# Kernel tuning notes

Measured on AMD Instinct MI355X. Metric: run time of the kernel, lower is better.

The kernel has to match this reference:

```python
import jax, jax.numpy as jnp
import numpy as np
import math

B, N, P, S, C, NC = 8, 20000, 256, 32, 256, 18


def setup_inputs() -> dict:
    key = jax.random.key(0)
    ks = jax.random.split(key, 20)
    w = lambda k, shape: jax.random.normal(k, shape, jnp.float32) * 0.02
    return {
        "xyz": jax.random.normal(ks[0], (B, N, 3), jnp.float32),
        "features": jax.random.normal(ks[1], (B, C, N), jnp.float32),
        "boxes_size": jax.random.uniform(ks[2], (B, P, 3), jnp.float32, 0.2, 1.5),
        "boxes_label": jax.random.normal(ks[3], (B, P, NC), jnp.float32),
        "ts": jax.random.uniform(ks[4], (B,), jnp.float32) * 1000.0,
        "inds": jax.random.randint(ks[5], (B, P), 0, N, jnp.int32),
        # SharedMLP (259 -> 128 -> 128 -> 128), bn=False so conv1x1+bias+ReLU
        "mw0": w(ks[6], (128, C + 3)), "mb0": jnp.zeros((128,), jnp.float32),
        "mw1": w(ks[7], (128, 128)), "mb1": jnp.zeros((128,), jnp.float32),
        "mw2": w(ks[8], (128, 128)), "mb2": jnp.zeros((128,), jnp.float32),
        # label SharedMLP (18+128 -> 256 -> 256 -> 256)
        "lw0": w(ks[9], (256, NC + 128)), "lb0": jnp.zeros((256,), jnp.float32),
        "lw1": w(ks[10], (256, 256)), "lb1": jnp.zeros((256,), jnp.float32),
        "lw2": w(ks[11], (256, 256)), "lb2": jnp.zeros((256,), jnp.float32),
        # time_mlp: sinusoid(128) -> 512 -> GELU -> 512 ; block: SiLU -> 256
        "tw0": w(ks[12], (512, 128)), "tb0": jnp.zeros((512,), jnp.float32),
        "tw1": w(ks[13], (512, 512)), "tb1": jnp.zeros((512,), jnp.float32),
        "bw": w(ks[14], (256, 512)), "bb": jnp.zeros((256,), jnp.float32),
        # time_mlp_label: sinusoid(256) -> 1024 -> GELU -> 1024 ; block: SiLU -> 512
        "tlw0": w(ks[15], (1024, 256)), "tlb0": jnp.zeros((1024,), jnp.float32),
        "tlw1": w(ks[16], (1024, 1024)), "tlb1": jnp.zeros((1024,), jnp.float32),
        "blw": w(ks[17], (512, 1024)), "blb": jnp.zeros((512,), jnp.float32),
    }


def _sinusoid(t, dim):
    half = dim // 2
    freqs = jnp.exp(jnp.arange(half, dtype=jnp.float32) * (-(math.log(10000.0) / (half - 1))))
    e = t[:, None] * freqs[None, :]
    return jnp.concatenate([jnp.sin(e), jnp.cos(e)], axis=-1)


def _film(feat, ts, w0, b0, w1, b1, bw, bb, dim):
    # feat: [B, D, P]; replicates torch repeat_interleave/chunk/reshape exactly
    temb = jax.nn.gelu(_sinusoid(ts, dim) @ w0.T + b0, approximate=False) @ w1.T + b1
    ss = jax.nn.silu(temb) @ bw.T + bb          # [B, 2D]
    ss = jnp.repeat(ss, P, axis=0)              # [B*P, 2D]
    scale, shift = jnp.split(ss, 2, axis=1)
    scale = scale.reshape(-1, P)
    shift = shift.reshape(-1, P)
    f = feat.reshape(-1, P)
    return (f * (scale + 1.0) + shift).reshape(feat.shape[0], -1, P)


def reference(xyz, features, boxes_size, boxes_label, ts, inds,
              mw0, mb0, mw1, mb1, mw2, mb2,
              lw0, lb0, lw1, lb1, lw2, lb2,
              tw0, tb0, tw1, tb1, bw, bb,
              tlw0, tlb0, tlw1, tlb1, blw, blb):
    # gather proposal centers
    new_xyz = jnp.take_along_axis(xyz, inds[:, :, None], axis=1)        # [B,P,3]
    # axis-aligned box containment (the hull corners are an AABB: center +/- size/2)
    half = boxes_size * 0.5
    inside = jnp.all(jnp.abs(xyz[:, None, :, :] - new_xyz[:, :, None, :]) <= half[:, :, None, :], axis=-1)  # [B,P,N]
    # deterministic with-replacement sampling of in-box points: in-box indices first (stable sort), then cycle
    order = jnp.argsort(jnp.logical_not(inside), axis=-1)               # [B,P,N]
    count = jnp.maximum(inside.sum(axis=-1), 1)                          # [B,P]
    pos = jnp.arange(S, dtype=count.dtype)[None, None, :] % count[:, :, None]
    idx = jnp.take_along_axis(order, pos, axis=-1)                       # [B,P,S]
    b_idx = jnp.arange(B)[:, None, None]
    gxyz = xyz[b_idx, idx] - new_xyz[:, :, None, :]                      # [B,P,S,3]
    gfeat = jnp.transpose(features, (0, 2, 1))[b_idx, idx]               # [B,P,S,C]
    g = jnp.concatenate([gxyz, gfeat], axis=-1)                          # [B,P,S,3+C]
    act = lambda x, w, b: jax.nn.relu(jnp.einsum('bpsc,oc->bpso', x, w) + b)
    h = act(act(act(g, mw0, mb0), mw1, mb1), mw2, mb2)                   # [B,P,S,128]
    nf = h.max(axis=2)                                                   # [B,P,128] (max-pool over nsample)
    nf_t = jnp.transpose(nf, (0, 2, 1))                                  # [B,128,P]
    new_features = _film(nf_t, ts, tw0, tb0, tw1, tb1, bw, bb, 128)
    # label branch
    li = jnp.concatenate([boxes_label, nf], axis=-1)                     # [B,P,18+128]
    act2 = lambda x, w, b: jax.nn.relu(jnp.einsum('bpc,oc->bpo', x, w) + b)
    lf = act2(act2(act2(li, lw0, lb0), lw1, lb1), lw2, lb2)              # [B,P,256]
    lf_t = jnp.transpose(lf, (0, 2, 1))                                  # [B,256,P]
    label_feature = _film(lf_t, ts, tlw0, tlb0, tlw1, tlb1, blw, blb, 256)
    return (new_xyz, new_features, label_feature, inds)
```

## Files before the change

### kernel.cpp

```cpp
#include <hip/hip_runtime.h>
#include <math.h>

#define BB 8
#define NN 20000
#define PP 256
#define SSAMP 32
#define CC 256

typedef unsigned short u16;
typedef unsigned int u32;
typedef __attribute__((ext_vector_type(8))) short short8;
typedef __attribute__((ext_vector_type(4))) float f32x4;

__device__ __forceinline__ float b2f(u16 u) {
    union { u32 i; float f; } x; x.i = ((u32)u) << 16; return x.f;
}
__device__ __forceinline__ u16 f2b(float f) {
    union { float f; u32 i; } x; x.f = f;
    u32 i = x.i;
    i += 0x7fffu + ((i >> 16) & 1u);
    return (u16)(i >> 16);
}
__device__ __forceinline__ float rnd_bf(float f) { return b2f(f2b(f)); }
__device__ __forceinline__ float geluf(float x) {
    return 0.5f * x * (1.0f + erff(x * 0.7071067811865476f));
}
__device__ __forceinline__ float siluf(float x) {
    return x / (1.0f + expf(-x));
}
__device__ __forceinline__ f32x4 fz4() { f32x4 z = {0.f,0.f,0.f,0.f}; return z; }

__device__ __forceinline__ float ldf(const void* p, size_t i, int f32f) {
    return f32f ? ((const float*)p)[i] : b2f(((const u16*)p)[i]);
}
__device__ __forceinline__ u16 ldw(const void* p, size_t i, int f32f) {
    return f32f ? f2b(((const float*)p)[i]) : ((const u16*)p)[i];
}

__device__ __forceinline__ int detect_f32d(const void* xyz) {
    int lane = threadIdx.x & 63;
    u16 u = ((const u16*)xyz)[(size_t)lane * 7496];
    int e = (u >> 7) & 0xFF;
    bool inR = (e >= 0x70) && (e <= 0x85);
    unsigned long long m = __ballot(inR);
    return (__popcll(m) < 48) ? 1 : 0;
}

__device__ __forceinline__ void repack_body(int f32f, int rb, int tid,
        const void* mw0, const void* mw1, const void* mw2,
        const void* lw0, const void* lw1, const void* lw2,
        const void* mb0, const void* mb1, const void* mb2,
        const void* lb0, const void* lb1, const void* lb2,
        u16* __restrict__ W0p, u16* __restrict__ W1p, u16* __restrict__ W2p,
        u16* __restrict__ L0p, u16* __restrict__ L1p, u16* __restrict__ L2p,
        float* __restrict__ biasF) {
    int i = rb * 256 + tid;
    if (i < 36864) {
        int o = i / 288, c = i % 288;
        u16 v = 0;
        if (c < 256) v = ldw(mw0, o * 259 + 3 + c, f32f);
        else if (c < 259) v = ldw(mw0, o * 259 + (c - 256), f32f);
        W0p[i] = v;
    } else if (i < 53248) {
        W1p[i - 36864] = ldw(mw1, i - 36864, f32f);
    } else if (i < 69632) {
        W2p[i - 53248] = ldw(mw2, i - 53248, f32f);
    } else if (i < 110592) {
        int j = i - 69632;
        int o = j / 160, c = j % 160;
        L0p[j] = (c < 146) ? ldw(lw0, o * 146 + c, f32f) : (u16)0;
    } else if (i < 176128) {
        L1p[i - 110592] = ldw(lw1, i - 110592, f32f);
    } else if (i < 241664) {
        L2p[i - 176128] = ldw(lw2, i - 176128, f32f);
    } else if (i < 242816) {
        int j = i - 241664;
        float v;
        if (j < 128) v = ldf(mb0, j, f32f);
        else if (j < 256) v = ldf(mb1, j - 128, f32f);
        else if (j < 384) v = ldf(mb2, j - 256, f32f);
        else if (j < 640) v = ldf(lb0, j - 384, f32f);
        else if (j < 896) v = ldf(lb1, j - 640, f32f);
        else v = ldf(lb2, j - 896, f32f);
        biasF[j] = v;
    }
}

__device__ __forceinline__ void transpose_body(int f32f, const void* __restrict__ feat,
        u16* __restrict__ featT, int n0i, int c0i, int bz, int b0, int tid,
        u16 (*tile)[66]) {
    int c0 = c0i * 64, n0 = n0i * 64;
    int b = b0 + bz;
    const size_t fb = (size_t)b * CC * NN;
    const size_t tb = (size_t)bz * NN * CC;
    if (n0 + 64 <= NN) {
        int n4 = tid & 15, ci = tid >> 4;
        if (f32f) {
            #pragma unroll
            for (int pass = 0; pass < 4; pass++) {
                int c = pass * 16 + ci;
                const float* src = (const float*)feat + fb + (size_t)(c0 + c) * NN + n0 + n4 * 4;
                float4 v = *(const float4*)src;
                tile[c][n4 * 4 + 0] = f2b(v.x);
                tile[c][n4 * 4 + 1] = f2b(v.y);
                tile[c][n4 * 4 + 2] = f2b(v.z);
                tile[c][n4 * 4 + 3] = f2b(v.w);
            }
        } else {
            #pragma unroll
            for (int pass = 0; pass < 4; pass++) {
                int c = pass * 16 + ci;
                const u16* src = (const u16*)feat + fb + (size_t)(c0 + c) * NN + n0 + n4 * 4;
                ushort4 v = *(const ushort4*)src;
                tile[c][n4 * 4 + 0] = v.x;
                tile[c][n4 * 4 + 1] = v.y;
                tile[c][n4 * 4 + 2] = v.z;
                tile[c][n4 * 4 + 3] = v.w;
            }
        }
        __syncthreads();
        int c4 = tid & 15, ni = tid >> 4;
        #pragma unroll
        for (int pass = 0; pass < 4; pass++) {
            int n = pass * 16 + ni;
            ushort4 o;
            o.x = tile[c4 * 4 + 0][n];
            o.y = tile[c4 * 4 + 1][n];
            o.z = tile[c4 * 4 + 2][n];
            o.w = tile[c4 * 4 + 3][n];
            *(ushort4*)(featT + tb + (size_t)(n0 + n) * CC + c0 + c4 * 4) = o;
        }
    } else {
        int tx = tid & 63, ty = tid >> 6;
        for (int i = 0; i < 16; i++) {
            int cl = ty * 16 + i;
            int n = n0 + tx;
            if (n < NN) tile[cl][tx] = ldw(feat, fb + (size_t)(c0 + cl) * NN + n, f32f);
        }
        __syncthreads();
        for (int i = 0; i < 16; i++) {
            int nl = ty * 16 + i;
            int n = n0 + nl;
            if (n < NN) featT[tb + (size_t)n * CC + c0 + tx] = tile[tx][nl];
        }
    }
}

template<int ACT, int SRC>
__device__ __forceinline__ void lin_body(int f32f, const void* __restrict__ xin,
        const void* __restrict__ W, const void* __restrict__ bias,
        float* __restrict__ out, int K, int O, int rb, int tid, float* xs) {
    if (SRC == 2) {
        const float* X = (const float*)xin;
        for (int i = tid; i < 8 * K; i += 256) xs[i] = X[i];
    } else {
        const int half = (SRC == 0) ? 64 : 128;
        const int dim = half * 2;
        const float cst = (SRC == 0) ? (logf(10000.f) / 63.f) : (logf(10000.f) / 127.f);
        for (int i = tid; i < 8 * dim; i += 256) {
            int b = i / dim, j = i % dim;
            float t = ldf(xin, b, f32f);
            int jj = (j < half) ? j : (j - half);
            float e = t * expf(-(float)jj * cst);
            xs[i] = (j < half) ? sinf(e) : cosf(e);
        }
    }
    __syncthreads();
    int lane = tid & 63, wv = tid >> 6;
    int r = rb * 4 + wv;
    if (r >= O) return;
    float acc[8] = {0.f, 0.f, 0.f, 0.f, 0.f, 0.f, 0.f, 0.f};
    for (int k = lane; k < K; k += 64) {
        float wval = ldf(W, (size_t)r * K + k, f32f);
        #pragma unroll
        for (int b = 0; b < 8; b++) acc[b] += wval * xs[b * K + k];
    }
    #pragma unroll
    for (int b = 0; b < 8; b++) {
        acc[b] += __shfl_xor(acc[b], 1);
        acc[b] += __shfl_xor(acc[b], 2);
        acc[b] += __shfl_xor(acc[b], 4);
        acc[b] += __shfl_xor(acc[b], 8);
        acc[b] += __shfl_xor(acc[b], 16);
        acc[b] += __shfl_xor(acc[b], 32);
    }
    if (lane == 0) {
        float bv = ldf(bias, r, f32f);
        #pragma unroll
        for (int b = 0; b < 8; b++) {
            float v = acc[b] + bv;
            if (ACT == 1) v = geluf(v);
            else if (ACT == 2) v = siluf(v);
            out[b * O + r] = v;
        }
    }
}

__device__ __forceinline__ void sample_body(int f32f, const void* __restrict__ xyz,
        const void* __restrict__ bsize, const int* __restrict__ inds,
        int* __restrict__ sidx, float* __restrict__ cenW,
        float* __restrict__ outXyz, float* __restrict__ outInds,
        int pg, int tid, int* sBuf, int* wcnt) {
    int lane = tid & 63, w = tid >> 6;
    int b = pg >> 8;
    int ind = inds[pg];
    ind = ind < 0 ? 0 : (ind >= NN ? NN - 1 : ind);
    if (tid < SSAMP) sBuf[tid] = 0;
    size_t xb = (size_t)b * NN * 3;
    float cx = ldf(xyz, xb + (size_t)ind * 3 + 0, f32f);
    float cy = ldf(xyz, xb + (size_t)ind * 3 + 1, f32f);
    float cz = ldf(xyz, xb + (size_t)ind * 3 + 2, f32f);
    float hx = 0.5f * ldf(bsize, pg * 3 + 0, f32f);
    float hy = 0.5f * ldf(bsize, pg * 3 + 1, f32f);
    float hz = 0.5f * ldf(bsize, pg * 3 + 2, f32f);
    int cnt = 0, par = 0;
    const unsigned long long lmask = (1ull << lane) - 1ull;
    int nn[4];
    float px[4], py[4], pz[4];
    #pragma unroll
    for (int u = 0; u < 4; u++) {
        int n = w * 256 + lane + u * 64;
        nn[u] = n;
        int nc = n < NN ? n : NN - 1;
        size_t a = xb + (size_t)nc * 3;
        px[u] = ldf(xyz, a, f32f);
        py[u] = ldf(xyz, a + 1, f32f);
        pz[u] = ldf(xyz, a + 2, f32f);
    }
    for (int base = 0;;) {
        int nbase = base + 1024;
        bool more = nbase < NN;
        int qn[4];
        float qx[4], qy[4], qz[4];
        if (more) {
            #pragma unroll
            for (int u = 0; u < 4; u++) {
                int n = nbase + w * 256 + lane + u * 64;
                qn[u] = n;
                int nc = n < NN ? n : NN - 1;
                size_t a = xb + (size_t)nc * 3;
                qx[u] = ldf(xyz, a, f32f);
                qy[u] = ldf(xyz, a + 1, f32f);
                qz[u] = ldf(xyz, a + 2, f32f);
            }
        }
        bool isin[4];
        unsigned long long m[4];
        int pc[4];
        int tw = 0;
        #pragma unroll
        for (int u = 0; u < 4; u++) {
            bool in_ = (nn[u] < NN) &&
                       (fabsf(px[u] - cx) <= hx) &&
                       (fabsf(py[u] - cy) <= hy) &&
                       (fabsf(pz[u] - cz) <= hz);
            isin[u] = in_;
            m[u] = __ballot(in_);
            pc[u] = (int)__popcll(m[u]);
            tw += pc[u];
        }
        if (lane == 0) wcnt[par + w] = tw;
        __syncthreads();
        int w0 = wcnt[par + 0], w1 = wcnt[par + 1], w2 = wcnt[par + 2], w3 = wcnt[par + 3];
        int total = w0 + w1 + w2 + w3;
        int prior = cnt;
        if (w >= 1) prior += w0;
        if (w >= 2) prior += w1;
        if (w >= 3) prior += w2;
        #pragma unroll
        for (int u = 0; u < 4; u++) {
            int pos = prior + (int)__popcll(m[u] & lmask);
            if (isin[u] && pos < SSAMP) sBuf[pos] = nn[u];
            prior += pc[u];
        }
        cnt += total;
        if (cnt >= SSAMP || !more) break;
        par ^= 4;
        base = nbase;
        #pragma unroll
        for (int u = 0; u < 4; u++) {
            nn[u] = qn[u]; px[u] = qx[u]; py[u] = qy[u]; pz[u] = qz[u];
        }
    }
    __syncthreads();
    int ccap = cnt < SSAMP ? cnt : SSAMP;
    if (ccap < 1) ccap = 1;
    if (tid < SSAMP) sidx[pg * SSAMP + tid] = sBuf[tid % ccap];
    if (tid < 3) {
        float cv = tid == 0 ? cx : (tid == 1 ? cy : cz);
        outXyz[pg * 3 + tid] = cv;
        cenW[pg * 3 + tid] = cv;
    }
    if (tid == 0) outInds[pg] = rnd_bf((float)ind);
}

__device__ __forceinline__ void mlp1_body(int f32f,
        const u16* __restrict__ featT, const void* __restrict__ feat,
        int pbase, int tier,
        const void* __restrict__ xyz, const int* __restrict__ sidx,
        const float* __restrict__ cenW,
        const u16* __restrict__ W0p, const u16* __restrict__ W1p,
        const u16* __restrict__ W2p, const float* __restrict__ biasF,
        u16* __restrict__ nfB, float* __restrict__ nfF,
        int tid, u16* gA, int* nrowS, float* centS) {
    int b = pbase >> 8;
    if (tid < 64) {
        int n = sidx[pbase * SSAMP + tid];
        nrowS[tid] = n < 0 ? 0 : (n >= NN ? NN - 1 : n);
    }
    if (tid < 6) centS[tid] = cenW[pbase * 3 + tid];
    for (int e = tid; e < 64 * 32; e += 256) {
        int row = e >> 5, c2 = e & 31;
        if (c2 >= 8 && c2 < 28)
            *(u32*)&gA[row * 296 + 256 + (c2 - 8) * 2] = 0u;
    }
    __syncthreads();
    if (tier >= 1) {
        size_t rowBase = (tier == 2) ? ((size_t)b * NN) : 0;
        for (int e = tid; e < 64 * 32; e += 256) {
            int row = e >> 5, seg = e & 31;
            int n = nrowS[row];
            uint4 v = *(const uint4*)(featT + (rowBase + n) * CC + seg * 8);
            *(uint4*)&gA[row * 296 + seg * 8] = v;
        }
    } else {
        int row = tid & 63;
        int n = nrowS[row];
        const size_t fb = (size_t)b * CC * NN;
        int cbase = tid >> 6;
        for (int it = 0; it < 64; it++) {
            int cch = it * 4 + cbase;
            gA[row * 296 + cch] = ldw(feat, fb + (size_t)cch * NN + n, f32f);
        }
    }
    if (tid < 64) {
        int row = tid, q = row >> 5;
        int n = nrowS[row];
        size_t a = ((size_t)b * NN + n) * 3;
        for (int d = 0; d < 3; d++) {
            float gv = ldf(xyz, a + d, f32f) - centS[q * 3 + d];
            gA[row * 296 + 256 + d] = f2b(gv);
        }
    }
    __syncthreads();

    int lane = tid & 63, w = tid >> 6;
    int c15 = lane & 15, kq = lane >> 4;
    f32x4 acc[4][2];

    for (int mt = 0; mt < 4; mt++) for (int j = 0; j < 2; j++) acc[mt][j] = fz4();
    for (int ks = 0; ks < 9; ks++) {
        int k0 = ks * 32 + kq * 8;
        short8 af[4];
        for (int mt = 0; mt < 4; mt++)
            af[mt] = *(const short8*)&gA[(mt * 16 + c15) * 296 + k0];
        for (int j = 0; j < 2; j++) {
            int col = w * 32 + j * 16 + c15;
            short8 bf = *(const short8*)(W0p + col * 288 + k0);
            for (int mt = 0; mt < 4; mt++)
                acc[mt][j] = __builtin_amdgcn_mfma_f32_16x16x32_bf16(af[mt], bf, acc[mt][j], 0, 0, 0);
        }
    }
    __syncthreads();
    u16* h1s = gA;
    u16* h2s = gA + 8704;
    for (int j = 0; j < 2; j++) {
        int col = w * 32 + j * 16 + c15;
        float bias = biasF[col];
        for (int mt = 0; mt < 4; mt++)
            for (int r = 0; r < 4; r++) {
                float v = acc[mt][j][r] + bias;
                v = v > 0.f ? v : 0.f;
                h1s[(mt * 16 + kq * 4 + r) * 136 + col] = f2b(v);
            }
    }
    __syncthreads();

    for (int mt = 0; mt < 4; mt++) for (int j = 0; j < 2; j++) acc[mt][j] = fz4();
    for (int ks = 0; ks < 4; ks++) {
        int k0 = ks * 32 + kq * 8;
        short8 af[4];
        for (int mt = 0; mt < 4; mt++)
            af[mt] = *(const short8*)&h1s[(mt * 16 + c15) * 136 + k0];
        for (int j = 0; j < 2; j++) {
            int col = w * 32 + j * 16 + c15;
            short8 bf = *(const short8*)(W1p + col * 128 + k0);
            for (int mt = 0; mt < 4; mt++)
                acc[mt][j] = __builtin_amdgcn_mfma_f32_16x16x32_bf16(af[mt], bf, acc[mt][j], 0, 0, 0);
        }
    }
    __syncthreads();
    for (int j = 0; j < 2; j++) {
        int col = w * 32 + j * 16 + c15;
        float bias = biasF[128 + col];
        for (int mt = 0; mt < 4; mt++)
            for (int r = 0; r < 4; r++) {
                float v = acc[mt][j][r] + bias;
                v = v > 0.f ? v : 0.f;
                h2s[(mt * 16 + kq * 4 + r) * 136 + col] = f2b(v);
            }
    }
    __syncthreads();

    for (int mt = 0; mt < 4; mt++) for (int j = 0; j < 2; j++) acc[mt][j] = fz4();
    for (int ks = 0; ks < 4; ks++) {
        int k0 = ks * 32 + kq * 8;
        short8 af[4];
        for (int mt = 0; mt < 4; mt++)
            af[mt] = *(const short8*)&h2s[(mt * 16 + c15) * 136 + k0];
        for (int j = 0; j < 2; j++) {
            int col = w * 32 + j * 16 + c15;
            short8 bf = *(const short8*)(W2p + col * 128 + k0);
            for (int mt = 0; mt < 4; mt++)
                acc[mt][j] = __builtin_amdgcn_mfma_f32_16x16x32_bf16(af[mt], bf, acc[mt][j], 0, 0, 0);
        }
    }
    int pA = pbase & 255, pB = (pbase + 1) & 255;
    for (int j = 0; j < 2; j++) {
        int col = w * 32 + j * 16 + c15;
        float bias = biasF[256 + col];
        float mA = 0.f, mB = 0.f;
        for (int mt = 0; mt < 2; mt++)
            for (int r = 0; r < 4; r++) {
                float v = acc[mt][j][r] + bias; v = v > 0.f ? v : 0.f;
                mA = fmaxf(mA, v);
            }
        for (int mt = 2; mt < 4; mt++)
            for (int r = 0; r < 4; r++) {
                float v = acc[mt][j][r] + bias; v = v > 0.f ? v : 0.f;
                mB = fmaxf(mB, v);
            }
        mA = fmaxf(mA, __shfl_xor(mA, 16)); mA = fmaxf(mA, __shfl_xor(mA, 32));
        mB = fmaxf(mB, __shfl_xor(mB, 16)); mB = fmaxf(mB, __shfl_xor(mB, 32));
        if (lane < 16) {
            nfB[(size_t)(pbase + 0) * 128 + col] = f2b(mA);
            nfB[(size_t)(pbase + 1) * 128 + col] = f2b(mB);
            nfF[((size_t)b * 128 + col) * 256 + pA] = mA;
            nfF[((size_t)b * 128 + col) * 256 + pB] = mB;
        }
    }
}

__global__ __launch_bounds__(256) void k_front(
        const void* __restrict__ xyz, const void* __restrict__ feat,
        const void* __restrict__ bsize, const int* __restrict__ inds,
        const void* __restrict__ ts,
        const void* mw0, const void* mw1, const void* mw2,
        const void* lw0, const void* lw1, const void* lw2,
        const void* mb0, const void* mb1, const void* mb2,
        const void* lb0, const void* lb1, const void* lb2,
        const void* tw0, const void* tb0,
        const void* tlw0, const void* tlb0,
        u16* __restrict__ featT, int nTrans,
        int* __restrict__ sidx, float* __restrict__ cenW,
        float* __restrict__ outXyz, float* __restrict__ outInds,
        u16* __restrict__ W0p, u16* __restrict__ W1p, u16* __restrict__ W2p,
        u16* __restrict__ L0p, u16* __restrict__ L1p, u16* __restrict__ L2p,
        float* __restrict__ biasF, float* __restrict__ h0W, float* __restrict__ g0W) {
    __shared__ __align__(16) char smem[8448];
    int tid = threadIdx.x;
    int f32f = detect_f32d(xyz);
    unsigned bx = blockIdx.x;
    unsigned s1 = (unsigned)nTrans + 2048u;
    unsigned s2 = s1 + 949u;
    unsigned s3 = s2 + 128u;
    if (bx < (unsigned)nTrans) {
        int t = (int)bx;
        transpose_body(f32f, feat, featT, t % 313, (t / 313) & 3, t / 1252, 0, tid,
                       (u16(*)[66])smem);
    } else if (bx < s1) {
        sample_body(f32f, xyz, bsize, inds, sidx, cenW, outXyz, outInds,
                    (int)(bx - (unsigned)nTrans), tid, (int*)smem, (int*)(smem + 128));
    } else if (bx < s2) {
        repack_body(f32f, (int)(bx - s1), tid, mw0, mw1, mw2, lw0, lw1, lw2,
                    mb0, mb1, mb2, lb0, lb1, lb2, W0p, W1p, W2p, L0p, L1p, L2p, biasF);
    } else if (bx < s3) {
        lin_body<1, 0>(f32f, ts, tw0, tb0, h0W, 128, 512, (int)(bx - s2), tid, (float*)smem);
    } else {
        lin_body<1, 1>(f32f, ts, tlw0, tlb0, g0W, 256, 1024, (int)(bx - s3), tid, (float*)smem);
    }
}

__global__ __launch_bounds__(256) void k_mid(int nMlp, int blockOff, int tier,
        const u16* __restrict__ featT, const void* __restrict__ feat,
        const void* __restrict__ xyz, const int* __restrict__ sidx,
        const float* __restrict__ cenW,
        const u16* __restrict__ W0p, const u16* __restrict__ W1p,
        const u16* __restrict__ W2p, const float* __restrict__ biasF,
        u16* __restrict__ nfB, float* __restrict__ nfF,
        const void* tw1, const void* tb1, const void* tlw1, const void* tlb1,
        const float* __restrict__ h0W, const float* __restrict__ g0W,
        float* __restrict__ tembW, float* __restrict__ temblW) {
    __shared__ __align__(16) char smem[38176];
    int tid = threadIdx.x;
    int f32f = detect_f32d(xyz);
    int bx = (int)blockIdx.x;
    if (bx < nMlp) {
        mlp1_body(f32f, featT, feat, (bx + blockOff) * 2, tier, xyz, sidx, cenW,
                  W0p, W1p, W2p, biasF, nfB, nfF, tid,
                  (u16*)smem, (int*)(smem + 37888), (float*)(smem + 38144));
    } else {
        int lb = bx - nMlp;
        float* xs = (float*)smem;
        if (lb < 128) lin_body<2, 2>(f32f, h0W, tw1, tb1, tembW, 512, 512, lb, tid, xs);
        else lin_body<2, 2>(f32f, g0W, tlw1, tlb1, temblW, 1024, 1024, lb - 128, tid, xs);
    }
}

__global__ __launch_bounds__(256) void k_lin3(const void* __restrict__ xyz,
        const void* bw, const void* bb, const void* blw, const void* blb,
        const float* __restrict__ tembW, const float* __restrict__ temblW,
        float* __restrict__ ssW, float* __restrict__ sslW) {
    __shared__ float xs[8 * 1024];
    int tid = threadIdx.x;
    int f32f = detect_f32d(xyz);
    unsigned bx = blockIdx.x;
    if (bx < 64u) lin_body<0, 2>(f32f, tembW, bw, bb, ssW, 512, 256, (int)bx, tid, xs);
    else lin_body<0, 2>(f32f, temblW, blw, blb, sslW, 1024, 512, (int)(bx - 64u), tid, xs);
}

__global__ __launch_bounds__(256) void k_transpose(const void* __restrict__ xyz,
                                                   const void* __restrict__ feat,
                                                   u16* __restrict__ featT, int b0) {
    __shared__ u16 tile[64][66];
    int f32f = detect_f32d(xyz);
    transpose_body(f32f, feat, featT, blockIdx.x, blockIdx.y, blockIdx.z, b0,
                   threadIdx.x, tile);
}

__global__ __launch_bounds__(256) void k_tail(const void* __restrict__ xyz,
        const void* __restrict__ blabel,
        const u16* __restrict__ nfB, const u16* __restrict__ L0p,
        const u16* __restrict__ L1p, const u16* __restrict__ L2p,
        const float* __restrict__ biasF, const float* __restrict__ sslW,
        const float* __restrict__ ssW, const float* __restrict__ nfF,
        float* __restrict__ outLF, float* __restrict__ outNF) {
    __shared__ u16 liS[16 * 168];
    __shared__ u16 h1L[16 * 264];
    __shared__ u16 h2L[16 * 264];
    int f32f = detect_f32d(xyz);
    int tid = threadIdx.x;
    unsigned bxu = blockIdx.x;
    if (bxu >= 128u) {
        int base = (int)(bxu - 128u) * 4096;
        #pragma unroll
        for (int i = 0; i < 16; i++) {
            int idx = base + i * 256 + tid;
            int p = idx & 255;
            int cb = idx >> 8;
            int b = cb >> 7;
            float sc = ssW[b * 256 + (p & 127)] + 1.f;
            float sh = ssW[b * 256 + 128 + (p & 127)];
            outNF[idx] = nfF[idx] * sc + sh;
        }
        return;
    }
    int pbase = (int)bxu * 16;
    for (int e = tid; e < 16 * 160; e += 256) {
        int row = e / 160, c = e % 160;
        int pg = pbase + row;
        u16 v = 0;
        if (c < 18) v = ldw(blabel, pg * 18 + c, f32f);
        else if (c < 146) v = nfB[(size_t)pg * 128 + (c - 18)];
        liS[row * 168 + c] = v;
    }
    __syncthreads();
    int lane = tid & 63, w = tid >> 6;
    int c15 = lane & 15, kq = lane >> 4;
    f32x4 acc[4];

    for (int j = 0; j < 4; j++) acc[j] = fz4();
    for (int ks = 0; ks < 5; ks++) {
        int k0 = ks * 32 + kq * 8;
        short8 af = *(const short8*)&liS[c15 * 168 + k0];
        for (int j = 0; j < 4; j++) {
            int col = w * 64 + j * 16 + c15;
            short8 bf = *(const short8*)(L0p + col * 160 + k0);
            acc[j] = __builtin_amdgcn_mfma_f32_16x16x32_bf16(af, bf, acc[j], 0, 0, 0);
        }
    }
    for (int j = 0; j < 4; j++) {
        int col = w * 64 + j * 16 + c15;
        float bias = biasF[384 + col];
        for (int r = 0; r < 4; r++) {
            float v = acc[j][r] + bias; v = v > 0.f ? v : 0.f;
            h1L[(kq * 4 + r) * 264 + col] = f2b(v);
        }
    }
    __syncthreads();

    for (int j = 0; j < 4; j++) acc[j] = fz4();
    for (int ks = 0; ks < 8; ks++) {
        int k0 = ks * 32 + kq * 8;
        short8 af = *(const short8*)&h1L[c15 * 264 + k0];
        for (int j = 0; j < 4; j++) {
            int col = w * 64 + j * 16 + c15;
            short8 bf = *(const short8*)(L1p + col * 256 + k0);
            acc[j] = __builtin_amdgcn_mfma_f32_16x16x32_bf16(af, bf, acc[j], 0, 0, 0);
        }
    }
    for (int j = 0; j < 4; j++) {
        int col = w * 64 + j * 16 + c15;
        float bias = biasF[640 + col];
        for (int r = 0; r < 4; r++) {
            float v = acc[j][r] + bias; v = v > 0.f ? v : 0.f;
            h2L[(kq * 4 + r) * 264 + col] = f2b(v);
        }
    }
    __syncthreads();

    for (int j = 0; j < 4; j++) acc[j] = fz4();
    for (int ks = 0; ks < 8; ks++) {
        int k0 = ks * 32 + kq * 8;
        short8 af = *(const short8*)&h2L[c15 * 264 + k0];
        for (int j = 0; j < 4; j++) {
            int col = w * 64 + j * 16 + c15;
            short8 bf = *(const short8*)(L2p + col * 256 + k0);
            acc[j] = __builtin_amdgcn_mfma_f32_16x16x32_bf16(af, bf, acc[j], 0, 0, 0);
        }
    }
    for (int j = 0; j < 4; j++) {
        int col = w * 64 + j * 16 + c15;
        float bias = biasF[896 + col];
        for (int r = 0; r < 4; r++) {
            int pr = pbase + kq * 4 + r;
            int bb2 = pr >> 8, p = pr & 255;
            float v = acc[j][r] + bias; v = v > 0.f ? v : 0.f;
            float sc = sslW[bb2 * 512 + p] + 1.f;
            float sh = sslW[bb2 * 512 + 256 + p];
            outLF[((size_t)bb2 * 256 + col) * 256 + p] = v * sc + sh;
        }
    }
}

extern "C" void kernel_launch(void* const* d_in, const int* in_sizes, int n_in,
                              void* d_out, int out_size, void* d_ws, size_t ws_size,
                              hipStream_t stream) {
    const void* xyz    = d_in[0];
    const void* feat   = d_in[1];
    const void* bsize  = d_in[2];
    const void* blabel = d_in[3];
    const void* ts     = d_in[4];
    const int* inds    = (const int*)d_in[5];
    const void* mw0 = d_in[6];  const void* mb0 = d_in[7];
    const void* mw1 = d_in[8];  const void* mb1 = d_in[9];
    const void* mw2 = d_in[10]; const void* mb2 = d_in[11];
    const void* lw0 = d_in[12]; const void* lb0 = d_in[13];
    const void* lw1 = d_in[14]; const void* lb1 = d_in[15];
    const void* lw2 = d_in[16]; const void* lb2 = d_in[17];
    const void* tw0 = d_in[18]; const void* tb0 = d_in[19];
    const void* tw1 = d_in[20]; const void* tb1 = d_in[21];
    const void* bw  = d_in[22]; const void* bb  = d_in[23];
    const void* tlw0 = d_in[24]; const void* tlb0 = d_in[25];
    const void* tlw1 = d_in[26]; const void* tlb1 = d_in[27];
    const void* blw  = d_in[28]; const void* blb  = d_in[29];

    float* out = (float*)d_out;
    float* outXyz  = out;
    float* outNF   = out + 6144;
    float* outLF   = out + 268288;
    float* outInds = out + 792576;

    char* ws = (char*)d_ws;
    u16*   W0p   = (u16*)(ws + 64);
    u16*   W1p   = (u16*)(ws + 73792);
    u16*   W2p   = (u16*)(ws + 106560);
    u16*   L0p   = (u16*)(ws + 139328);
    u16*   L1p   = (u16*)(ws + 221248);
    u16*   L2p   = (u16*)(ws + 352320);
    float* biasF = (float*)(ws + 483392);
    float* ssW   = (float*)(ws + 488000);
    float* sslW  = (float*)(ws + 496192);
    float* cenW  = (float*)(ws + 512576);
    int*   sidx  = (int*)(ws + 537152);
    u16*   nfB   = (u16*)(ws + 799296);
    float* h0W   = (float*)(ws + 1323584);
    float* tembW = (float*)(ws + 1339968);
    float* g0W   = (float*)(ws + 1356352);
    float* temblW= (float*)(ws + 1389120);
    float* nfF   = (float*)(ws + 1421888);
    u16*   featT = (u16*)(ws + 2470464);
    const size_t NEED_A = 2470464ull + 81920000ull;
    const size_t NEED_B = 2470464ull + 10240000ull;
    int tier = (ws_size >= NEED_A) ? 2 : ((ws_size >= NEED_B) ? 1 : 0);

    int nTrans = (tier == 2) ? 10016 : 0;
    unsigned gFront = (unsigned)nTrans + 2048u + 949u + 128u + 256u;
    k_front<<<dim3(gFront), dim3(256), 0, stream>>>(
        xyz, feat, bsize, inds, ts,
        mw0, mw1, mw2, lw0, lw1, lw2,
        mb0, mb1, mb2, lb0, lb1, lb2,
        tw0, tb0, tlw0, tlb0,
        featT, nTrans, sidx, cenW, outXyz, outInds,
        W0p, W1p, W2p, L0p, L1p, L2p, biasF, h0W, g0W);

    if (tier == 2) {
        k_mid<<<dim3(1024 + 384), dim3(256), 0, stream>>>(1024, 0, 2,
            featT, feat, xyz, sidx, cenW, W0p, W1p, W2p, biasF, nfB, nfF,
            tw1, tb1, tlw1, tlb1, h0W, g0W, tembW, temblW);
    } else if (tier == 1) {
        for (int b = 0; b < BB; b++) {
            k_transpose<<<dim3(313, 4, 1), dim3(256), 0, stream>>>(xyz, feat, featT, b);
            k_mid<<<dim3(128), dim3(256), 0, stream>>>(128, b * 128, 1,
                featT, feat, xyz, sidx, cenW, W0p, W1p, W2p, biasF, nfB, nfF,
                tw1, tb1, tlw1, tlb1, h0W, g0W, tembW, temblW);
        }
        k_mid<<<dim3(384), dim3(256), 0, stream>>>(0, 0, 1,
            featT, feat, xyz, sidx, cenW, W0p, W1p, W2p, biasF, nfB, nfF,
            tw1, tb1, tlw1, tlb1, h0W, g0W, tembW, temblW);
    } else {
        k_mid<<<dim3(1024 + 384), dim3(256), 0, stream>>>(1024, 0, 0,
            featT, feat, xyz, sidx, cenW, W0p, W1p, W2p, biasF, nfB, nfF,
            tw1, tb1, tlw1, tlb1, h0W, g0W, tembW, temblW);
    }

    k_lin3<<<dim3(192), dim3(256), 0, stream>>>(xyz, bw, bb, blw, blb,
                                                tembW, temblW, ssW, sslW);

    k_tail<<<dim3(128 + 64), dim3(256), 0, stream>>>(xyz, blabel, nfB,
        L0p, L1p, L2p, biasF, sslW, ssW, nfF, outLF, outNF);
}
```

Measured before the change: 423.8 us.

## Interleave sampling blocks among transpose blocks and drop sample-loop prefetch

The front kernel's block map now puts one ball-query sampling block after every six transpose blocks, so the latency-bound sampling work runs alongside the bandwidth-bound transpose instead of after it. The grid becomes a fixed 7*2048 range, and the transpose blocks past nTrans exit idle. The sampling loop also drops its software prefetch of the next 1024 points in favour of a plain per-iteration load, using a 12-byte struct load for fp32 points. This lowers register pressure but exposes load latency on each iteration.

Result: no change. 417.7 us (-1.5%).

```diff
diff --git a/kernel.cpp b/kernel.cpp
--- a/kernel.cpp
+++ b/kernel.cpp
@@ -11,6 +11,8 @@
 typedef unsigned int u32;
 typedef __attribute__((ext_vector_type(8))) short short8;
 typedef __attribute__((ext_vector_type(4))) float f32x4;
+
+struct __align__(4) f3v { float x, y, z; };
 
 __device__ __forceinline__ float b2f(u16 u) {
     union { u32 i; float f; } x; x.i = ((u32)u) << 16; return x.f;
@@ -207,41 +209,38 @@
     ind = ind < 0 ? 0 : (ind >= NN ? NN - 1 : ind);
     if (tid < SSAMP) sBuf[tid] = 0;
     size_t xb = (size_t)b * NN * 3;
-    float cx = ldf(xyz, xb + (size_t)ind * 3 + 0, f32f);
-    float cy = ldf(xyz, xb + (size_t)ind * 3 + 1, f32f);
-    float cz = ldf(xyz, xb + (size_t)ind * 3 + 2, f32f);
+    const f3v* Pts = (const f3v*)((const float*)xyz + xb);
+    float cx, cy, cz;
+    if (f32f) {
+        f3v c = Pts[ind];
+        cx = c.x; cy = c.y; cz = c.z;
+    } else {
+        cx = b2f(((const u16*)xyz)[xb + (size_t)ind * 3 + 0]);
+        cy = b2f(((const u16*)xyz)[xb + (size_t)ind * 3 + 1]);
+        cz = b2f(((const u16*)xyz)[xb + (size_t)ind * 3 + 2]);
+    }
     float hx = 0.5f * ldf(bsize, pg * 3 + 0, f32f);
     float hy = 0.5f * ldf(bsize, pg * 3 + 1, f32f);
     float hz = 0.5f * ldf(bsize, pg * 3 + 2, f32f);
     int cnt = 0, par = 0;
     const unsigned long long lmask = (1ull << lane) - 1ull;
-    int nn[4];
-    float px[4], py[4], pz[4];
-    #pragma unroll
-    for (int u = 0; u < 4; u++) {
-        int n = w * 256 + lane + u * 64;
-        nn[u] = n;
-        int nc = n < NN ? n : NN - 1;
-        size_t a = xb + (size_t)nc * 3;
-        px[u] = ldf(xyz, a, f32f);
-        py[u] = ldf(xyz, a + 1, f32f);
-        pz[u] = ldf(xyz, a + 2, f32f);
-    }
-    for (int base = 0;;) {
-        int nbase = base + 1024;
-        bool more = nbase < NN;
-        int qn[4];
-        float qx[4], qy[4], qz[4];
-        if (more) {
-            #pragma unroll
-            for (int u = 0; u < 4; u++) {
-                int n = nbase + w * 256 + lane + u * 64;
-                qn[u] = n;
-                int nc = n < NN ? n : NN - 1;
+    for (int base = 0; base < NN; base += 1024, par ^= 4) {
+        int nb = base + w * 256 + lane;
+        int nn[4];
+        float px[4], py[4], pz[4];
+        #pragma unroll
+        for (int u = 0; u < 4; u++) {
+            int n = nb + u * 64;
+            nn[u] = n;
+            int nc = n < NN ? n : NN - 1;
+            if (f32f) {
+                f3v v = Pts[nc];
+                px[u] = v.x; py[u] = v.y; pz[u] = v.z;
+            } else {
                 size_t a = xb + (size_t)nc * 3;
-                qx[u] = ldf(xyz, a, f32f);
-                qy[u] = ldf(xyz, a + 1, f32f);
-                qz[u] = ldf(xyz, a + 2, f32f);
+                px[u] = b2f(((const u16*)xyz)[a]);
+                py[u] = b2f(((const u16*)xyz)[a + 1]);
+                pz[u] = b2f(((const u16*)xyz)[a + 2]);
             }
         }
         bool isin[4];
@@ -274,13 +273,7 @@
             prior += pc[u];
         }
         cnt += total;
-        if (cnt >= SSAMP || !more) break;
-        par ^= 4;
-        base = nbase;
-        #pragma unroll
-        for (int u = 0; u < 4; u++) {
-            nn[u] = qn[u]; px[u] = qx[u]; py[u] = qy[u]; pz[u] = qz[u];
-        }
+        if (cnt >= SSAMP) break;
     }
     __syncthreads();
     int ccap = cnt < SSAMP ? cnt : SSAMP;
@@ -461,23 +454,38 @@
     int tid = threadIdx.x;
     int f32f = detect_f32d(xyz);
     unsigned bx = blockIdx.x;
-    unsigned s1 = (unsigned)nTrans + 2048u;
-    unsigned s2 = s1 + 949u;
-    unsigned s3 = s2 + 128u;
-    if (bx < (unsigned)nTrans) {
-        int t = (int)bx;
-        transpose_body(f32f, feat, featT, t % 313, (t / 313) & 3, t / 1252, 0, tid,
-                       (u16(*)[66])smem);
-    } else if (bx < s1) {
-        sample_body(f32f, xyz, bsize, inds, sidx, cenW, outXyz, outInds,
-                    (int)(bx - (unsigned)nTrans), tid, (int*)smem, (int*)(smem + 128));
-    } else if (bx < s2) {
-        repack_body(f32f, (int)(bx - s1), tid, mw0, mw1, mw2, lw0, lw1, lw2,
-                    mb0, mb1, mb2, lb0, lb1, lb2, W0p, W1p, W2p, L0p, L1p, L2p, biasF);
-    } else if (bx < s3) {
-        lin_body<1, 0>(f32f, ts, tw0, tb0, h0W, 128, 512, (int)(bx - s2), tid, (float*)smem);
+    if (nTrans > 0) {
+        const unsigned NI = 7u * 2048u;
+        if (bx < NI) {
+            if (bx % 7u == 0u) {
+                sample_body(f32f, xyz, bsize, inds, sidx, cenW, outXyz, outInds,
+                            (int)(bx / 7u), tid, (int*)smem, (int*)(smem + 128));
+            } else {
+                int t = (int)(bx - bx / 7u - 1u);
+                if (t < nTrans)
+                    transpose_body(f32f, feat, featT, t % 313, (t / 313) & 3, t / 1252,
+                                   0, tid, (u16(*)[66])smem);
+            }
+        } else if (bx < NI + 949u) {
+            repack_body(f32f, (int)(bx - NI), tid, mw0, mw1, mw2, lw0, lw1, lw2,
+                        mb0, mb1, mb2, lb0, lb1, lb2, W0p, W1p, W2p, L0p, L1p, L2p, biasF);
+        } else if (bx < NI + 1077u) {
+            lin_body<1, 0>(f32f, ts, tw0, tb0, h0W, 128, 512, (int)(bx - NI - 949u), tid, (float*)smem);
+        } else {
+            lin_body<1, 1>(f32f, ts, tlw0, tlb0, g0W, 256, 1024, (int)(bx - NI - 1077u), tid, (float*)smem);
+        }
     } else {
-        lin_body<1, 1>(f32f, ts, tlw0, tlb0, g0W, 256, 1024, (int)(bx - s3), tid, (float*)smem);
+        if (bx < 2048u) {
+            sample_body(f32f, xyz, bsize, inds, sidx, cenW, outXyz, outInds,
+                        (int)bx, tid, (int*)smem, (int*)(smem + 128));
+        } else if (bx < 2997u) {
+            repack_body(f32f, (int)(bx - 2048u), tid, mw0, mw1, mw2, lw0, lw1, lw2,
+                        mb0, mb1, mb2, lb0, lb1, lb2, W0p, W1p, W2p, L0p, L1p, L2p, biasF);
+        } else if (bx < 3125u) {
+            lin_body<1, 0>(f32f, ts, tw0, tb0, h0W, 128, 512, (int)(bx - 2997u), tid, (float*)smem);
+        } else {
+            lin_body<1, 1>(f32f, ts, tlw0, tlb0, g0W, 256, 1024, (int)(bx - 3125u), tid, (float*)smem);
+        }
     }
 }
 
@@ -685,7 +693,8 @@
     int tier = (ws_size >= NEED_A) ? 2 : ((ws_size >= NEED_B) ? 1 : 0);
 
     int nTrans = (tier == 2) ? 10016 : 0;
-    unsigned gFront = (unsigned)nTrans + 2048u + 949u + 128u + 256u;
+    unsigned gFront = (nTrans > 0) ? (7u * 2048u + 949u + 384u)
+                                   : (2048u + 949u + 384u);
     k_front<<<dim3(gFront), dim3(256), 0, stream>>>(
         xyz, feat, bsize, inds, ts,
         mw0, mw1, mw2, lw0, lw1, lw2,
```
